# Optimization experiments

Measured on AMD Instinct MI355X. Metric: run time of the kernel, lower is better.

## Reference

```python
import jax, jax.numpy as jnp
import numpy as np

ATOL = 1e-06
RTOL = 1e-06

def setup_inputs() -> dict:
    key = jax.random.key(0)
    ks = jax.random.split(key, 8)
    u = lambda k, shape: jax.random.uniform(k, shape, jnp.float32, -0.05, 0.05)
    return {
        "x": jax.random.normal(ks[0], (4096, 32, 32, 3), jnp.float32),
        "W_lstm": u(ks[1], (3, 16)),      # input kernel, gates [i,f,c,o]
        "U_lstm": u(ks[2], (4, 16)),      # recurrent kernel
        "dw_kernel": u(ks[3], (27, 27, 3, 5)),  # depthwise (kh,kw,in_c,mult)
        "pw_kernel": u(ks[4], (15, 4)),   # pointwise
        "conv_bias": u(ks[5], (4,)),
        "W_td": u(ks[6], (4096, 10)),
        "W_sc": u(ks[7], (4096, 10)),
    }

def _lstm_td(x, W, U):
    # TimeDistributed LSTM: x (B,32,32,3) -> treat axis1 as TD batch, axis2 as time
    B = x.shape[0]
    seq = x.reshape(B * 32, 32, 3)          # (N, T, F)
    xs = jnp.transpose(seq, (1, 0, 2))      # (T, N, F)
    N = seq.shape[0]
    h0 = jnp.zeros((N, 4), x.dtype)
    c0 = jnp.zeros((N, 4), x.dtype)

    def step(carry, xt):
        h, c = carry
        z = xt @ W + h @ U                  # (N, 16)
        zi, zf, zc, zo = jnp.split(z, 4, axis=-1)
        i = jax.nn.elu(zi)                  # recurrent_activation='elu'
        f = jax.nn.elu(zf)
        c = f * c + i * jax.nn.softmax(zc, axis=-1)  # activation='softmax'
        o = jax.nn.elu(zo)
        h = o * jax.nn.softmax(c, axis=-1)
        return (h, c), h

    _, hs = jax.lax.scan(step, (h0, c0), xs)        # (T, N, 4)
    return jnp.transpose(hs, (1, 0, 2)).reshape(B, 32, 32, 4)

def _sep_conv(x, dw_kernel, pw_kernel, conv_bias):
    # depthwise: Keras (kh,kw,C,M) -> lax HWIO grouped (kh,kw,1,C*M), channel-major order
    dw = dw_kernel.reshape(27, 27, 1, 15)
    y = jax.lax.conv_general_dilated(
        x, dw, window_strides=(1, 1), padding='SAME',
        feature_group_count=3,
        dimension_numbers=('NHWC', 'HWIO', 'NHWC'))   # (B,32,32,15)
    y = jnp.einsum('bhwc,cf->bhwf', y, pw_kernel) + conv_bias
    return jax.nn.sigmoid(y)                          # (B,32,32,4)

def reference(x, W_lstm, U_lstm, dw_kernel, pw_kernel, conv_bias, W_td, W_sc):
    B = x.shape[0]
    td = _lstm_td(x, W_lstm, U_lstm).reshape(B, -1) @ W_td   # (B,10)
    sc = _sep_conv(x, dw_kernel, pw_kernel, conv_bias).reshape(B, -1) @ W_sc
    diff = jnp.abs(td - sc)
    tol = ATOL + RTOL * jnp.abs(sc)
    return diff <= tol
```

## Files before the change

kernel.cpp:

```cpp
#include <hip/hip_runtime.h>
#include <math.h>

#define TD_OFF 0
#define WTDR_OFF 40960
#define BG_BYTE_OFF 524288

typedef __bf16 bf16x8 __attribute__((ext_vector_type(8)));
typedef float f32x16 __attribute__((ext_vector_type(16)));

union FragU { bf16x8 v; float4 f; };

__device__ __forceinline__ f32x16 mfma16(bf16x8 a, bf16x8 b, f32x16 c) {
    return __builtin_amdgcn_mfma_f32_32x32x16_bf16(a, b, c, 0, 0, 0);
}

__device__ __forceinline__ float eluf(float v) {
    return v > 0.f ? v : __expf(v) - 1.f;
}

__global__ __launch_bounds__(256) void lstm_prep(const float* __restrict__ x,
                                                 const float* __restrict__ W,
                                                 const float* __restrict__ U,
                                                 const float* __restrict__ Wtd,
                                                 const float* __restrict__ dw,
                                                 const float* __restrict__ pw,
                                                 float* __restrict__ Wtdr,
                                                 unsigned short* __restrict__ Bg,
                                                 float* __restrict__ td_out) {
    int t = threadIdx.x;
    if (blockIdx.x >= 512) {
        int gid = (blockIdx.x - 512) * 256 + t;
        if (gid < 40960) {
            int k = gid & 3;
            int r = gid >> 2;
            int j = r % 10; r /= 10;
            int row = r & 31;
            int tt = r >> 5;
            Wtdr[gid] = Wtd[(size_t)(row * 128 + tt * 4 + k) * 10 + j];
            return;
        }
        int g2 = gid - 40960;
        if (g2 >= 162 * 128) return;
        int n = g2 & 127;
        int s = g2 >> 7;
        int half = s & 1;
        int cd = s >> 1;
        int c = cd / 27, d = cd % 27;
        int w = n >> 2, f = n & 3;
        unsigned short* dsth = Bg + (size_t)s * 4096 + n * 16;
        unsigned short* dstl = dsth + 2048;
#pragma unroll
        for (int k = 0; k < 16; k++) {
            int xi = half * 16 + k;
            int dx = xi - w + 13;
            float v = 0.f;
            if (dx >= 0 && dx < 27) {
#pragma unroll
                for (int m = 0; m < 5; m++)
                    v = fmaf(dw[((d * 27 + dx) * 3 + c) * 5 + m],
                             pw[(c * 5 + m) * 4 + f], v);
            }
            __bf16 h = (__bf16)v;
            __bf16 l = (__bf16)(v - (float)h);
            dsth[k] = __builtin_bit_cast(unsigned short, h);
            dstl[k] = __builtin_bit_cast(unsigned short, l);
        }
        return;
    }

    float rW[48], rU[64];
    const float4* W4 = (const float4*)W;
    const float4* U4 = (const float4*)U;
#pragma unroll
    for (int i = 0; i < 12; i++) {
        float4 q = W4[i];
        rW[i * 4 + 0] = q.x; rW[i * 4 + 1] = q.y;
        rW[i * 4 + 2] = q.z; rW[i * 4 + 3] = q.w;
    }
#pragma unroll
    for (int i = 0; i < 16; i++) {
        float4 q = U4[i];
        rU[i * 4 + 0] = q.x; rU[i * 4 + 1] = q.y;
        rU[i * 4 + 2] = q.z; rU[i * 4 + 3] = q.w;
    }

    int n = blockIdx.x * 256 + t;
    int row = n & 31;
    const float4* xp4 = (const float4*)(x + (size_t)n * 96);

    float h0 = 0, h1 = 0, h2 = 0, h3 = 0;
    float c0 = 0, c1 = 0, c2 = 0, c3 = 0;
    float acc[10];
#pragma unroll
    for (int j = 0; j < 10; j++) acc[j] = 0.f;

    for (int g = 0; g < 8; g++) {
        float4 q0 = xp4[g * 3 + 0], q1 = xp4[g * 3 + 1], q2 = xp4[g * 3 + 2];
        float xr[12] = {q0.x, q0.y, q0.z, q0.w, q1.x, q1.y,
                        q1.z, q1.w, q2.x, q2.y, q2.z, q2.w};
#pragma unroll
        for (int st = 0; st < 4; st++) {
            int tt = g * 4 + st;
            float x0 = xr[st * 3 + 0], x1 = xr[st * 3 + 1], x2 = xr[st * 3 + 2];
            float z[16];
#pragma unroll
            for (int k = 0; k < 16; k++)
                z[k] = x0 * rW[k] + x1 * rW[16 + k] + x2 * rW[32 + k]
                     + h0 * rU[k] + h1 * rU[16 + k] + h2 * rU[32 + k] + h3 * rU[48 + k];

            float ig0 = eluf(z[0]),  ig1 = eluf(z[1]),  ig2 = eluf(z[2]),  ig3 = eluf(z[3]);
            float fg0 = eluf(z[4]),  fg1 = eluf(z[5]),  fg2 = eluf(z[6]),  fg3 = eluf(z[7]);
            float og0 = eluf(z[12]), og1 = eluf(z[13]), og2 = eluf(z[14]), og3 = eluf(z[15]);

            float zm = fmaxf(fmaxf(z[8], z[9]), fmaxf(z[10], z[11]));
            float e0 = __expf(z[8] - zm), e1 = __expf(z[9] - zm);
            float e2 = __expf(z[10] - zm), e3 = __expf(z[11] - zm);
            float inv = 1.f / (e0 + e1 + e2 + e3);
            c0 = fg0 * c0 + ig0 * (e0 * inv);
            c1 = fg1 * c1 + ig1 * (e1 * inv);
            c2 = fg2 * c2 + ig2 * (e2 * inv);
            c3 = fg3 * c3 + ig3 * (e3 * inv);

            float cm = fmaxf(fmaxf(c0, c1), fmaxf(c2, c3));
            float p0 = __expf(c0 - cm), p1 = __expf(c1 - cm);
            float p2 = __expf(c2 - cm), p3 = __expf(c3 - cm);
            float pinv = 1.f / (p0 + p1 + p2 + p3);
            h0 = og0 * (p0 * pinv); h1 = og1 * (p1 * pinv);
            h2 = og2 * (p2 * pinv); h3 = og3 * (p3 * pinv);

            const float4* wr4 = (const float4*)(Wtdr + (size_t)(tt * 32 + row) * 40);
#pragma unroll
            for (int j = 0; j < 10; j++) {
                float4 q = wr4[j];
                acc[j] += h0 * q.x + h1 * q.y + h2 * q.z + h3 * q.w;
            }
        }
    }

#pragma unroll
    for (int off = 16; off >= 1; off >>= 1) {
#pragma unroll
        for (int j = 0; j < 10; j++) acc[j] += __shfl_xor(acc[j], off, 64);
    }
    int lane = t & 63;
    if (lane == 0 || lane == 32) {
        int b = n >> 5;
#pragma unroll
        for (int j = 0; j < 10; j++) td_out[b * 10 + j] = acc[j];
    }
}

#define A_OFF 0
#define ZOFF 24576
#define SRED_OFF 24592
#define LDS_BYTES 24912

__global__ __launch_bounds__(256, 4) void conv_sc(const float* __restrict__ x,
                                                  const unsigned short* __restrict__ Bg,
                                                  const float* __restrict__ Wsc,
                                                  const float* __restrict__ bias,
                                                  const float* __restrict__ td,
                                                  float* __restrict__ out) {
    __shared__ char LDS[LDS_BYTES] __attribute__((aligned(16)));
    int t = threadIdx.x;
    int l = t & 63;
    int wv = t >> 6;
    int m = l & 31;
    int sub = l >> 5;

    const char* bbase = (const char*)Bg + (size_t)wv * 1024 + m * 32 + sub * 16;
    FragU bufA[2], bufB[2], bufC[2];
#define LOADB(sv, arr) { const char* p_ = bbase + (size_t)(sv) * 8192;       \
        arr[0].f = *(const float4*)(p_);                                     \
        arr[1].f = *(const float4*)(p_ + 4096); }

    LOADB(0, bufA);
    LOADB(1, bufB);

    const float4* xb4 = (const float4*)(x + (size_t)blockIdx.x * 6144);
#pragma unroll
    for (int it = 0; it < 6; it++) {
        int fi = it * 256 + t;
        float4 q = xb4[fi];
        float vals[4] = {q.x, q.y, q.z, q.w};
#pragma unroll
        for (int e = 0; e < 4; e++) {
            int pel = fi * 4 + e;
            int img = pel / 3072;
            int p = pel - img * 3072;
            int c = p % 3;
            int hw = p / 3;
            int w = hw & 31;
            int h = hw >> 5;
            int rec = A_OFF + (((img * 3 + c) * 8) + (w >> 4) * 2 + ((w >> 3) & 1)) * 512
                      + h * 16 + (w & 7) * 2;
            float v = vals[e];
            __bf16 hb = (__bf16)v;
            __bf16 lb = (__bf16)(v - (float)hb);
            *(__bf16*)(LDS + rec) = hb;
            *(__bf16*)(LDS + rec + 2048) = lb;
        }
    }
    if (t < 4) *(float*)(LDS + ZOFF + t * 4) = 0.f;
    __syncthreads();

    f32x16 acc0 = {0,0,0,0,0,0,0,0,0,0,0,0,0,0,0,0};
    f32x16 acc1 = acc0;

    int c = 0, d = 0, half = 0;

#define CHUNK(USE, DST, SNEXT) {                                              \
    LOADB(SNEXT, DST);                                                        \
    int rowIdx = m + d - 13;                                                  \
    bool valid = (unsigned)rowIdx < 32u;                                      \
    int a0 = A_OFF + (c * 8 + half * 2 + sub) * 512 + rowIdx * 16;            \
    int ah0o = valid ? a0 : ZOFF;                                             \
    int al0o = valid ? (a0 + 2048) : ZOFF;                                    \
    int ah1o = valid ? (a0 + 12288) : ZOFF;                                   \
    int al1o = valid ? (a0 + 14336) : ZOFF;                                   \
    FragU ah0, al0, ah1, al1;                                                 \
    ah0.f = *(const float4*)(LDS + ah0o);                                     \
    al0.f = *(const float4*)(LDS + al0o);                                     \
    ah1.f = *(const float4*)(LDS + ah1o);                                     \
    al1.f = *(const float4*)(LDS + al1o);                                     \
    acc0 = mfma16(ah0.v, USE[0].v, acc0);                                     \
    acc1 = mfma16(ah1.v, USE[0].v, acc1);                                     \
    acc0 = mfma16(ah0.v, USE[1].v, acc0);                                     \
    acc1 = mfma16(ah1.v, USE[1].v, acc1);                                     \
    acc0 = mfma16(al0.v, USE[0].v, acc0);                                     \
    acc1 = mfma16(al1.v, USE[0].v, acc1);                                     \
    half ^= 1;                                                                \
    if (!half) { d++; if (d == 27) { d = 0; c++; } }                          \
}

    for (int g = 0; g < 54; g++) {
        CHUNK(bufA, bufC, 3 * g + 2);
        CHUNK(bufB, bufA, 3 * g + 3);
        CHUNK(bufC, bufB, 3 * g + 4);
    }

    float b4[4];
#pragma unroll
    for (int i = 0; i < 4; i++) b4[i] = bias[i];

    float part[2][10];
#pragma unroll
    for (int i = 0; i < 2; i++)
#pragma unroll
        for (int j = 0; j < 10; j++) part[i][j] = 0.f;

    f32x16 accs[2] = {acc0, acc1};
#pragma unroll
    for (int i2 = 0; i2 < 2; i2++) {
        int ncol = wv * 32 + m;
        int wcol = ncol >> 2;
        int f = ncol & 3;
        f32x16 a = accs[i2];
#pragma unroll
        for (int r = 0; r < 16; r++) {
            int h = (r & 3) + 8 * (r >> 2) + 4 * sub;
            float v = a[r] + b4[f];
            float sg = 1.f / (1.f + expf(-v));
            const float* wr = Wsc + (size_t)((h * 32 + wcol) * 4 + f) * 10;
#pragma unroll
            for (int j = 0; j < 10; j++) part[i2][j] = fmaf(sg, wr[j], part[i2][j]);
        }
    }

#pragma unroll
    for (int off = 32; off >= 1; off >>= 1) {
#pragma unroll
        for (int i2 = 0; i2 < 2; i2++)
#pragma unroll
            for (int j = 0; j < 10; j++) part[i2][j] += __shfl_xor(part[i2][j], off, 64);
    }
    if (l == 0) {
        float* red = (float*)(LDS + SRED_OFF);
#pragma unroll
        for (int i2 = 0; i2 < 2; i2++)
#pragma unroll
            for (int j = 0; j < 10; j++) red[(wv * 2 + i2) * 10 + j] = part[i2][j];
    }
    __syncthreads();
    if (t < 20) {
        int i2 = t / 10, j = t % 10;
        const float* red = (const float*)(LDS + SRED_OFF);
        float sv = red[(0 * 2 + i2) * 10 + j] + red[(1 * 2 + i2) * 10 + j]
                 + red[(2 * 2 + i2) * 10 + j] + red[(3 * 2 + i2) * 10 + j];
        int oi = (blockIdx.x * 2 + i2) * 10 + j;
        float a = td[oi];
        float tol = 1e-6f + 1e-6f * fabsf(sv);
        out[oi] = (fabsf(a - sv) <= tol) ? 1.0f : 0.0f;
    }
}

extern "C" void kernel_launch(void* const* d_in, const int* in_sizes, int n_in,
                              void* d_out, int out_size, void* d_ws, size_t ws_size,
                              hipStream_t stream) {
    const float* x    = (const float*)d_in[0];
    const float* W    = (const float*)d_in[1];
    const float* U    = (const float*)d_in[2];
    const float* dw   = (const float*)d_in[3];
    const float* pw   = (const float*)d_in[4];
    const float* bias = (const float*)d_in[5];
    const float* Wtd  = (const float*)d_in[6];
    const float* Wsc  = (const float*)d_in[7];

    float* ws     = (float*)d_ws;
    float* td_acc = ws + TD_OFF;
    float* Wtdr   = ws + WTDR_OFF;
    unsigned short* Bg = (unsigned short*)((char*)d_ws + BG_BYTE_OFF);

    lstm_prep<<<753, 256, 0, stream>>>(x, W, U, Wtd, dw, pw, Wtdr, Bg, td_acc);
    conv_sc<<<2048, 256, 0, stream>>>(x, Bg, Wsc, bias, td_acc, (float*)d_out);
}
```

Measured before the change: 400.0 us.

## Split LSTM into own kernel with LDS-staged input and remap conv MFMA tiles

Splits the old fused prep kernel into a weight-prep kernel and a separate LSTM kernel. The LSTM kernel runs 64-thread blocks and stages x through padded LDS, so per-thread strided global loads become coalesced. The conv kernel now gives each wave one image and two N-tiles instead of two images and one N-tile, which halves A-fragment LDS reads per wave. It also moves to double-buffered B loads issued after the MFMAs and raises the launch-bounds occupancy hint from 4 to 5. The trade-offs are an extra launch, a serial dependence between prep and the LSTM, and more B-fragment register and global-load pressure per wave.

Result: slower. 507.6 us (+26.9%).

```diff
diff --git a/kernel.cpp b/kernel.cpp
--- a/kernel.cpp
+++ b/kernel.cpp
@@ -18,55 +18,66 @@
     return v > 0.f ? v : __expf(v) - 1.f;
 }
 
-__global__ __launch_bounds__(256) void lstm_prep(const float* __restrict__ x,
-                                                 const float* __restrict__ W,
-                                                 const float* __restrict__ U,
-                                                 const float* __restrict__ Wtd,
-                                                 const float* __restrict__ dw,
-                                                 const float* __restrict__ pw,
-                                                 float* __restrict__ Wtdr,
-                                                 unsigned short* __restrict__ Bg,
-                                                 float* __restrict__ td_out) {
+__global__ __launch_bounds__(256) void prep(const float* __restrict__ dw,
+                                            const float* __restrict__ pw,
+                                            const float* __restrict__ Wtd,
+                                            float* __restrict__ Wtdr,
+                                            unsigned short* __restrict__ Bg) {
+    int gid = blockIdx.x * 256 + threadIdx.x;
+    if (gid < 40960) {
+        int k = gid & 3;
+        int r = gid >> 2;
+        int j = r % 10; r /= 10;
+        int row = r & 31;
+        int tt = r >> 5;
+        Wtdr[gid] = Wtd[(size_t)(row * 128 + tt * 4 + k) * 10 + j];
+        return;
+    }
+    int g2 = gid - 40960;
+    if (g2 >= 162 * 128) return;
+    int n = g2 & 127;
+    int s = g2 >> 7;
+    int half = s & 1;
+    int cd = s >> 1;
+    int c = cd / 27, d = cd % 27;
+    int w = n >> 2, f = n & 3;
+    unsigned short* dsth = Bg + (size_t)s * 4096 + n * 16;
+    unsigned short* dstl = dsth + 2048;
+#pragma unroll
+    for (int k = 0; k < 16; k++) {
+        int xi = half * 16 + k;
+        int dx = xi - w + 13;
+        float v = 0.f;
+        if (dx >= 0 && dx < 27) {
+#pragma unroll
+            for (int m = 0; m < 5; m++)
+                v = fmaf(dw[((d * 27 + dx) * 3 + c) * 5 + m],
+                         pw[(c * 5 + m) * 4 + f], v);
+        }
+        __bf16 h = (__bf16)v;
+        __bf16 l = (__bf16)(v - (float)h);
+        dsth[k] = __builtin_bit_cast(unsigned short, h);
+        dstl[k] = __builtin_bit_cast(unsigned short, l);
+    }
+}
+
+__global__ __launch_bounds__(64) void lstm_td(const float* __restrict__ x,
+                                              const float* __restrict__ W,
+                                              const float* __restrict__ U,
+                                              const float* __restrict__ Wtdr,
+                                              float* __restrict__ td_out) {
+    __shared__ float4 xls[64 * 25];
     int t = threadIdx.x;
-    if (blockIdx.x >= 512) {
-        int gid = (blockIdx.x - 512) * 256 + t;
-        if (gid < 40960) {
-            int k = gid & 3;
-            int r = gid >> 2;
-            int j = r % 10; r /= 10;
-            int row = r & 31;
-            int tt = r >> 5;
-            Wtdr[gid] = Wtd[(size_t)(row * 128 + tt * 4 + k) * 10 + j];
-            return;
-        }
-        int g2 = gid - 40960;
-        if (g2 >= 162 * 128) return;
-        int n = g2 & 127;
-        int s = g2 >> 7;
-        int half = s & 1;
-        int cd = s >> 1;
-        int c = cd / 27, d = cd % 27;
-        int w = n >> 2, f = n & 3;
-        unsigned short* dsth = Bg + (size_t)s * 4096 + n * 16;
-        unsigned short* dstl = dsth + 2048;
-#pragma unroll
-        for (int k = 0; k < 16; k++) {
-            int xi = half * 16 + k;
-            int dx = xi - w + 13;
-            float v = 0.f;
-            if (dx >= 0 && dx < 27) {
-#pragma unroll
-                for (int m = 0; m < 5; m++)
-                    v = fmaf(dw[((d * 27 + dx) * 3 + c) * 5 + m],
-                             pw[(c * 5 + m) * 4 + f], v);
-            }
-            __bf16 h = (__bf16)v;
-            __bf16 l = (__bf16)(v - (float)h);
-            dsth[k] = __builtin_bit_cast(unsigned short, h);
-            dstl[k] = __builtin_bit_cast(unsigned short, l);
-        }
-        return;
-    }
+
+    const float4* xb4 = (const float4*)(x + (size_t)blockIdx.x * 64 * 96);
+#pragma unroll
+    for (int i = 0; i < 24; i++) {
+        int fidx = i * 64 + t;
+        int seq = fidx / 24;
+        int e = fidx - seq * 24;
+        xls[seq * 25 + e] = xb4[fidx];
+    }
+    __syncthreads();
 
     float rW[48], rU[64];
     const float4* W4 = (const float4*)W;
@@ -84,9 +95,8 @@
         rU[i * 4 + 2] = q.z; rU[i * 4 + 3] = q.w;
     }
 
-    int n = blockIdx.x * 256 + t;
+    int n = blockIdx.x * 64 + t;
     int row = n & 31;
-    const float4* xp4 = (const float4*)(x + (size_t)n * 96);
 
     float h0 = 0, h1 = 0, h2 = 0, h3 = 0;
     float c0 = 0, c1 = 0, c2 = 0, c3 = 0;
@@ -95,7 +105,9 @@
     for (int j = 0; j < 10; j++) acc[j] = 0.f;
 
     for (int g = 0; g < 8; g++) {
-        float4 q0 = xp4[g * 3 + 0], q1 = xp4[g * 3 + 1], q2 = xp4[g * 3 + 2];
+        float4 q0 = xls[t * 25 + g * 3 + 0];
+        float4 q1 = xls[t * 25 + g * 3 + 1];
+        float4 q2 = xls[t * 25 + g * 3 + 2];
         float xr[12] = {q0.x, q0.y, q0.z, q0.w, q1.x, q1.y,
                         q1.z, q1.w, q2.x, q2.y, q2.z, q2.w};
 #pragma unroll
@@ -142,8 +154,7 @@
 #pragma unroll
         for (int j = 0; j < 10; j++) acc[j] += __shfl_xor(acc[j], off, 64);
     }
-    int lane = t & 63;
-    if (lane == 0 || lane == 32) {
+    if (t == 0 || t == 32) {
         int b = n >> 5;
 #pragma unroll
         for (int j = 0; j < 10; j++) td_out[b * 10 + j] = acc[j];
@@ -153,9 +164,9 @@
 #define A_OFF 0
 #define ZOFF 24576
 #define SRED_OFF 24592
-#define LDS_BYTES 24912
-
-__global__ __launch_bounds__(256, 4) void conv_sc(const float* __restrict__ x,
+#define LDS_BYTES 24752
+
+__global__ __launch_bounds__(256, 5) void conv_sc(const float* __restrict__ x,
                                                   const unsigned short* __restrict__ Bg,
                                                   const float* __restrict__ Wsc,
                                                   const float* __restrict__ bias,
@@ -167,12 +178,16 @@
     int wv = t >> 6;
     int m = l & 31;
     int sub = l >> 5;
-
-    const char* bbase = (const char*)Bg + (size_t)wv * 1024 + m * 32 + sub * 16;
-    FragU bufA[2], bufB[2], bufC[2];
+    int img = wv >> 1;
+    int ntbase = (wv & 1) * 2;
+
+    const char* bbase = (const char*)Bg + (size_t)(ntbase * 32 + m) * 32 + sub * 16;
+    FragU bufA[4], bufB[4];
 #define LOADB(sv, arr) { const char* p_ = bbase + (size_t)(sv) * 8192;       \
-        arr[0].f = *(const float4*)(p_);                                     \
-        arr[1].f = *(const float4*)(p_ + 4096); }
+        arr[0].f = *(const float4*)(p_);                         \
+        arr[1].f = *(const float4*)(p_ + 4096);                  \
+        arr[2].f = *(const float4*)(p_ + 1024);                  \
+        arr[3].f = *(const float4*)(p_ + 5120); }
 
     LOADB(0, bufA);
     LOADB(1, bufB);
@@ -186,13 +201,13 @@
 #pragma unroll
         for (int e = 0; e < 4; e++) {
             int pel = fi * 4 + e;
-            int img = pel / 3072;
-            int p = pel - img * 3072;
+            int im = pel / 3072;
+            int p = pel - im * 3072;
             int c = p % 3;
             int hw = p / 3;
             int w = hw & 31;
             int h = hw >> 5;
-            int rec = A_OFF + (((img * 3 + c) * 8) + (w >> 4) * 2 + ((w >> 3) & 1)) * 512
+            int rec = A_OFF + (((im * 3 + c) * 8) + (w >> 4) * 2 + ((w >> 3) & 1)) * 512
                       + h * 16 + (w & 7) * 2;
             float v = vals[e];
             __bf16 hb = (__bf16)v;
@@ -208,54 +223,48 @@
     f32x16 acc1 = acc0;
 
     int c = 0, d = 0, half = 0;
-
-#define CHUNK(USE, DST, SNEXT) {                                              \
-    LOADB(SNEXT, DST);                                                        \
+    int aimg = A_OFF + img * 12288;
+
+#define CHUNK(USE, SNEXT) {                                                   \
     int rowIdx = m + d - 13;                                                  \
     bool valid = (unsigned)rowIdx < 32u;                                      \
-    int a0 = A_OFF + (c * 8 + half * 2 + sub) * 512 + rowIdx * 16;            \
-    int ah0o = valid ? a0 : ZOFF;                                             \
-    int al0o = valid ? (a0 + 2048) : ZOFF;                                    \
-    int ah1o = valid ? (a0 + 12288) : ZOFF;                                   \
-    int al1o = valid ? (a0 + 14336) : ZOFF;                                   \
-    FragU ah0, al0, ah1, al1;                                                 \
-    ah0.f = *(const float4*)(LDS + ah0o);                                     \
-    al0.f = *(const float4*)(LDS + al0o);                                     \
-    ah1.f = *(const float4*)(LDS + ah1o);                                     \
-    al1.f = *(const float4*)(LDS + al1o);                                     \
-    acc0 = mfma16(ah0.v, USE[0].v, acc0);                                     \
-    acc1 = mfma16(ah1.v, USE[0].v, acc1);                                     \
-    acc0 = mfma16(ah0.v, USE[1].v, acc0);                                     \
-    acc1 = mfma16(ah1.v, USE[1].v, acc1);                                     \
-    acc0 = mfma16(al0.v, USE[0].v, acc0);                                     \
-    acc1 = mfma16(al1.v, USE[0].v, acc1);                                     \
+    int a0 = aimg + (c * 8 + half * 2 + sub) * 512 + rowIdx * 16;             \
+    int aho = valid ? a0 : ZOFF;                                              \
+    int alo = valid ? (a0 + 2048) : ZOFF;                                     \
+    FragU ah, al;                                                             \
+    ah.f = *(const float4*)(LDS + aho);                                       \
+    al.f = *(const float4*)(LDS + alo);                                       \
+    acc0 = mfma16(ah.v, USE[0].v, acc0);                                      \
+    acc1 = mfma16(ah.v, USE[2].v, acc1);                                      \
+    acc0 = mfma16(ah.v, USE[1].v, acc0);                                      \
+    acc1 = mfma16(ah.v, USE[3].v, acc1);                                      \
+    acc0 = mfma16(al.v, USE[0].v, acc0);                                      \
+    acc1 = mfma16(al.v, USE[2].v, acc1);                                      \
+    LOADB(SNEXT, USE);                                                        \
     half ^= 1;                                                                \
     if (!half) { d++; if (d == 27) { d = 0; c++; } }                          \
 }
 
-    for (int g = 0; g < 54; g++) {
-        CHUNK(bufA, bufC, 3 * g + 2);
-        CHUNK(bufB, bufA, 3 * g + 3);
-        CHUNK(bufC, bufB, 3 * g + 4);
+    for (int g = 0; g < 81; g++) {
+        CHUNK(bufA, 2 * g + 2);
+        CHUNK(bufB, 2 * g + 3);
     }
 
     float b4[4];
 #pragma unroll
     for (int i = 0; i < 4; i++) b4[i] = bias[i];
 
-    float part[2][10];
-#pragma unroll
-    for (int i = 0; i < 2; i++)
-#pragma unroll
-        for (int j = 0; j < 10; j++) part[i][j] = 0.f;
+    float part[10];
+#pragma unroll
+    for (int j = 0; j < 10; j++) part[j] = 0.f;
 
     f32x16 accs[2] = {acc0, acc1};
 #pragma unroll
-    for (int i2 = 0; i2 < 2; i2++) {
-        int ncol = wv * 32 + m;
+    for (int j2 = 0; j2 < 2; j2++) {
+        int ncol = (ntbase + j2) * 32 + m;
         int wcol = ncol >> 2;
         int f = ncol & 3;
-        f32x16 a = accs[i2];
+        f32x16 a = accs[j2];
 #pragma unroll
         for (int r = 0; r < 16; r++) {
             int h = (r & 3) + 8 * (r >> 2) + 4 * sub;
@@ -263,30 +272,25 @@
             float sg = 1.f / (1.f + expf(-v));
             const float* wr = Wsc + (size_t)((h * 32 + wcol) * 4 + f) * 10;
 #pragma unroll
-            for (int j = 0; j < 10; j++) part[i2][j] = fmaf(sg, wr[j], part[i2][j]);
+            for (int j = 0; j < 10; j++) part[j] = fmaf(sg, wr[j], part[j]);
         }
     }
 
 #pragma unroll
     for (int off = 32; off >= 1; off >>= 1) {
 #pragma unroll
-        for (int i2 = 0; i2 < 2; i2++)
-#pragma unroll
-            for (int j = 0; j < 10; j++) part[i2][j] += __shfl_xor(part[i2][j], off, 64);
+        for (int j = 0; j < 10; j++) part[j] += __shfl_xor(part[j], off, 64);
     }
     if (l == 0) {
         float* red = (float*)(LDS + SRED_OFF);
 #pragma unroll
-        for (int i2 = 0; i2 < 2; i2++)
-#pragma unroll
-            for (int j = 0; j < 10; j++) red[(wv * 2 + i2) * 10 + j] = part[i2][j];
+        for (int j = 0; j < 10; j++) red[wv * 10 + j] = part[j];
     }
     __syncthreads();
     if (t < 20) {
         int i2 = t / 10, j = t % 10;
         const float* red = (const float*)(LDS + SRED_OFF);
-        float sv = red[(0 * 2 + i2) * 10 + j] + red[(1 * 2 + i2) * 10 + j]
-                 + red[(2 * 2 + i2) * 10 + j] + red[(3 * 2 + i2) * 10 + j];
+        float sv = red[(i2 * 2) * 10 + j] + red[(i2 * 2 + 1) * 10 + j];
         int oi = (blockIdx.x * 2 + i2) * 10 + j;
         float a = td[oi];
         float tol = 1e-6f + 1e-6f * fabsf(sv);
@@ -311,6 +315,7 @@
     float* Wtdr   = ws + WTDR_OFF;
     unsigned short* Bg = (unsigned short*)((char*)d_ws + BG_BYTE_OFF);
 
-    lstm_prep<<<753, 256, 0, stream>>>(x, W, U, Wtd, dw, pw, Wtdr, Bg, td_acc);
+    prep<<<241, 256, 0, stream>>>(dw, pw, Wtd, Wtdr, Bg);
+    lstm_td<<<2048, 64, 0, stream>>>(x, W, U, Wtdr, td_acc);
     conv_sc<<<2048, 256, 0, stream>>>(x, Bg, Wsc, bias, td_acc, (float*)d_out);
 }
```

## Run LSTM blocks concurrently with conv blocks in one fused launch

Applied to the files above, without the earlier changes.

Splits the weight-prep work into its own small kernel, then merges the LSTM recurrence blocks and the separable-conv MFMA blocks into one grid so the two independent branches run side by side on the GPU. LSTM weights now come from LDS instead of registers. A third tiny kernel does the final tolerance compare, since the conv blocks can no longer read the LSTM result directly. This adds one extra launch and routes the conv result through global memory, and the LSTM blocks inherit the conv kernel's launch bounds and LDS footprint.

Result: slower. 456.4 us (+14.1%).

```diff
diff --git a/kernel.cpp b/kernel.cpp
--- a/kernel.cpp
+++ b/kernel.cpp
@@ -2,7 +2,8 @@
 #include <math.h>
 
 #define TD_OFF 0
-#define WTDR_OFF 40960
+#define SC_OFF 40960
+#define WTDR_OFF 81920
 #define BG_BYTE_OFF 524288
 
 typedef __bf16 bf16x8 __attribute__((ext_vector_type(8)));
@@ -18,151 +19,141 @@
     return v > 0.f ? v : __expf(v) - 1.f;
 }
 
-__global__ __launch_bounds__(256) void lstm_prep(const float* __restrict__ x,
-                                                 const float* __restrict__ W,
-                                                 const float* __restrict__ U,
-                                                 const float* __restrict__ Wtd,
-                                                 const float* __restrict__ dw,
-                                                 const float* __restrict__ pw,
-                                                 float* __restrict__ Wtdr,
-                                                 unsigned short* __restrict__ Bg,
-                                                 float* __restrict__ td_out) {
-    int t = threadIdx.x;
-    if (blockIdx.x >= 512) {
-        int gid = (blockIdx.x - 512) * 256 + t;
-        if (gid < 40960) {
-            int k = gid & 3;
-            int r = gid >> 2;
-            int j = r % 10; r /= 10;
-            int row = r & 31;
-            int tt = r >> 5;
-            Wtdr[gid] = Wtd[(size_t)(row * 128 + tt * 4 + k) * 10 + j];
-            return;
-        }
-        int g2 = gid - 40960;
-        if (g2 >= 162 * 128) return;
-        int n = g2 & 127;
-        int s = g2 >> 7;
-        int half = s & 1;
-        int cd = s >> 1;
-        int c = cd / 27, d = cd % 27;
-        int w = n >> 2, f = n & 3;
-        unsigned short* dsth = Bg + (size_t)s * 4096 + n * 16;
-        unsigned short* dstl = dsth + 2048;
-#pragma unroll
-        for (int k = 0; k < 16; k++) {
-            int xi = half * 16 + k;
-            int dx = xi - w + 13;
-            float v = 0.f;
-            if (dx >= 0 && dx < 27) {
-#pragma unroll
-                for (int m = 0; m < 5; m++)
-                    v = fmaf(dw[((d * 27 + dx) * 3 + c) * 5 + m],
-                             pw[(c * 5 + m) * 4 + f], v);
-            }
-            __bf16 h = (__bf16)v;
-            __bf16 l = (__bf16)(v - (float)h);
-            dsth[k] = __builtin_bit_cast(unsigned short, h);
-            dstl[k] = __builtin_bit_cast(unsigned short, l);
-        }
+__global__ __launch_bounds__(256) void prep(const float* __restrict__ dw,
+                                            const float* __restrict__ pw,
+                                            const float* __restrict__ Wtd,
+                                            float* __restrict__ Wtdr,
+                                            unsigned short* __restrict__ Bg) {
+    int gid = blockIdx.x * 256 + threadIdx.x;
+    if (gid < 40960) {
+        int k = gid & 3;
+        int r = gid >> 2;
+        int j = r % 10; r /= 10;
+        int row = r & 31;
+        int tt = r >> 5;
+        Wtdr[gid] = Wtd[(size_t)(row * 128 + tt * 4 + k) * 10 + j];
         return;
     }
-
-    float rW[48], rU[64];
-    const float4* W4 = (const float4*)W;
-    const float4* U4 = (const float4*)U;
-#pragma unroll
-    for (int i = 0; i < 12; i++) {
-        float4 q = W4[i];
-        rW[i * 4 + 0] = q.x; rW[i * 4 + 1] = q.y;
-        rW[i * 4 + 2] = q.z; rW[i * 4 + 3] = q.w;
-    }
-#pragma unroll
-    for (int i = 0; i < 16; i++) {
-        float4 q = U4[i];
-        rU[i * 4 + 0] = q.x; rU[i * 4 + 1] = q.y;
-        rU[i * 4 + 2] = q.z; rU[i * 4 + 3] = q.w;
-    }
-
-    int n = blockIdx.x * 256 + t;
-    int row = n & 31;
-    const float4* xp4 = (const float4*)(x + (size_t)n * 96);
-
-    float h0 = 0, h1 = 0, h2 = 0, h3 = 0;
-    float c0 = 0, c1 = 0, c2 = 0, c3 = 0;
-    float acc[10];
-#pragma unroll
-    for (int j = 0; j < 10; j++) acc[j] = 0.f;
-
-    for (int g = 0; g < 8; g++) {
-        float4 q0 = xp4[g * 3 + 0], q1 = xp4[g * 3 + 1], q2 = xp4[g * 3 + 2];
-        float xr[12] = {q0.x, q0.y, q0.z, q0.w, q1.x, q1.y,
-                        q1.z, q1.w, q2.x, q2.y, q2.z, q2.w};
-#pragma unroll
-        for (int st = 0; st < 4; st++) {
-            int tt = g * 4 + st;
-            float x0 = xr[st * 3 + 0], x1 = xr[st * 3 + 1], x2 = xr[st * 3 + 2];
-            float z[16];
-#pragma unroll
-            for (int k = 0; k < 16; k++)
-                z[k] = x0 * rW[k] + x1 * rW[16 + k] + x2 * rW[32 + k]
-                     + h0 * rU[k] + h1 * rU[16 + k] + h2 * rU[32 + k] + h3 * rU[48 + k];
-
-            float ig0 = eluf(z[0]),  ig1 = eluf(z[1]),  ig2 = eluf(z[2]),  ig3 = eluf(z[3]);
-            float fg0 = eluf(z[4]),  fg1 = eluf(z[5]),  fg2 = eluf(z[6]),  fg3 = eluf(z[7]);
-            float og0 = eluf(z[12]), og1 = eluf(z[13]), og2 = eluf(z[14]), og3 = eluf(z[15]);
-
-            float zm = fmaxf(fmaxf(z[8], z[9]), fmaxf(z[10], z[11]));
-            float e0 = __expf(z[8] - zm), e1 = __expf(z[9] - zm);
-            float e2 = __expf(z[10] - zm), e3 = __expf(z[11] - zm);
-            float inv = 1.f / (e0 + e1 + e2 + e3);
-            c0 = fg0 * c0 + ig0 * (e0 * inv);
-            c1 = fg1 * c1 + ig1 * (e1 * inv);
-            c2 = fg2 * c2 + ig2 * (e2 * inv);
-            c3 = fg3 * c3 + ig3 * (e3 * inv);
-
-            float cm = fmaxf(fmaxf(c0, c1), fmaxf(c2, c3));
-            float p0 = __expf(c0 - cm), p1 = __expf(c1 - cm);
-            float p2 = __expf(c2 - cm), p3 = __expf(c3 - cm);
-            float pinv = 1.f / (p0 + p1 + p2 + p3);
-            h0 = og0 * (p0 * pinv); h1 = og1 * (p1 * pinv);
-            h2 = og2 * (p2 * pinv); h3 = og3 * (p3 * pinv);
-
-            const float4* wr4 = (const float4*)(Wtdr + (size_t)(tt * 32 + row) * 40);
-#pragma unroll
-            for (int j = 0; j < 10; j++) {
-                float4 q = wr4[j];
-                acc[j] += h0 * q.x + h1 * q.y + h2 * q.z + h3 * q.w;
-            }
-        }
-    }
-
-#pragma unroll
-    for (int off = 16; off >= 1; off >>= 1) {
-#pragma unroll
-        for (int j = 0; j < 10; j++) acc[j] += __shfl_xor(acc[j], off, 64);
-    }
-    int lane = t & 63;
-    if (lane == 0 || lane == 32) {
-        int b = n >> 5;
-#pragma unroll
-        for (int j = 0; j < 10; j++) td_out[b * 10 + j] = acc[j];
+    int g2 = gid - 40960;
+    if (g2 >= 162 * 128) return;
+    int n = g2 & 127;
+    int s = g2 >> 7;
+    int half = s & 1;
+    int cd = s >> 1;
+    int c = cd / 27, d = cd % 27;
+    int w = n >> 2, f = n & 3;
+    unsigned short* dsth = Bg + (size_t)s * 4096 + n * 16;
+    unsigned short* dstl = dsth + 2048;
+#pragma unroll
+    for (int k = 0; k < 16; k++) {
+        int xi = half * 16 + k;
+        int dx = xi - w + 13;
+        float v = 0.f;
+        if (dx >= 0 && dx < 27) {
+#pragma unroll
+            for (int m = 0; m < 5; m++)
+                v = fmaf(dw[((d * 27 + dx) * 3 + c) * 5 + m],
+                         pw[(c * 5 + m) * 4 + f], v);
+        }
+        __bf16 h = (__bf16)v;
+        __bf16 l = (__bf16)(v - (float)h);
+        dsth[k] = __builtin_bit_cast(unsigned short, h);
+        dstl[k] = __builtin_bit_cast(unsigned short, l);
     }
 }
 
 #define A_OFF 0
 #define ZOFF 24576
 #define SRED_OFF 24592
-#define LDS_BYTES 24912
-
-__global__ __launch_bounds__(256, 4) void conv_sc(const float* __restrict__ x,
-                                                  const unsigned short* __restrict__ Bg,
-                                                  const float* __restrict__ Wsc,
-                                                  const float* __restrict__ bias,
-                                                  const float* __restrict__ td,
-                                                  float* __restrict__ out) {
+#define LDS_BYTES 24752
+
+__global__ __launch_bounds__(256, 4) void fused(const float* __restrict__ x,
+                                                const float* __restrict__ W,
+                                                const float* __restrict__ U,
+                                                const float* __restrict__ Wtdr,
+                                                const unsigned short* __restrict__ Bg,
+                                                const float* __restrict__ Wsc,
+                                                const float* __restrict__ bias,
+                                                float* __restrict__ td_out,
+                                                float* __restrict__ sc_out) {
     __shared__ char LDS[LDS_BYTES] __attribute__((aligned(16)));
     int t = threadIdx.x;
+
+    if (blockIdx.x < 512) {
+        float* sW = (float*)LDS;
+        float* sU = (float*)LDS + 48;
+        if (t < 48) sW[t] = W[t];
+        else if (t < 112) sU[t - 48] = U[t - 48];
+        __syncthreads();
+
+        int n = blockIdx.x * 256 + t;
+        int row = n & 31;
+        const float4* xp4 = (const float4*)(x + (size_t)n * 96);
+
+        float h0 = 0, h1 = 0, h2 = 0, h3 = 0;
+        float c0 = 0, c1 = 0, c2 = 0, c3 = 0;
+        float acc[10];
+#pragma unroll
+        for (int j = 0; j < 10; j++) acc[j] = 0.f;
+
+        for (int g = 0; g < 8; g++) {
+            float4 q0 = xp4[g * 3 + 0], q1 = xp4[g * 3 + 1], q2 = xp4[g * 3 + 2];
+            float xr[12] = {q0.x, q0.y, q0.z, q0.w, q1.x, q1.y,
+                            q1.z, q1.w, q2.x, q2.y, q2.z, q2.w};
+#pragma unroll
+            for (int st = 0; st < 4; st++) {
+                int tt = g * 4 + st;
+                float x0 = xr[st * 3 + 0], x1 = xr[st * 3 + 1], x2 = xr[st * 3 + 2];
+                float z[16];
+#pragma unroll
+                for (int k = 0; k < 16; k++)
+                    z[k] = x0 * sW[k] + x1 * sW[16 + k] + x2 * sW[32 + k]
+                         + h0 * sU[k] + h1 * sU[16 + k] + h2 * sU[32 + k] + h3 * sU[48 + k];
+
+                float ig0 = eluf(z[0]),  ig1 = eluf(z[1]),  ig2 = eluf(z[2]),  ig3 = eluf(z[3]);
+                float fg0 = eluf(z[4]),  fg1 = eluf(z[5]),  fg2 = eluf(z[6]),  fg3 = eluf(z[7]);
+                float og0 = eluf(z[12]), og1 = eluf(z[13]), og2 = eluf(z[14]), og3 = eluf(z[15]);
+
+                float zm = fmaxf(fmaxf(z[8], z[9]), fmaxf(z[10], z[11]));
+                float e0 = __expf(z[8] - zm), e1 = __expf(z[9] - zm);
+                float e2 = __expf(z[10] - zm), e3 = __expf(z[11] - zm);
+                float inv = 1.f / (e0 + e1 + e2 + e3);
+                c0 = fg0 * c0 + ig0 * (e0 * inv);
+                c1 = fg1 * c1 + ig1 * (e1 * inv);
+                c2 = fg2 * c2 + ig2 * (e2 * inv);
+                c3 = fg3 * c3 + ig3 * (e3 * inv);
+
+                float cm = fmaxf(fmaxf(c0, c1), fmaxf(c2, c3));
+                float p0 = __expf(c0 - cm), p1 = __expf(c1 - cm);
+                float p2 = __expf(c2 - cm), p3 = __expf(c3 - cm);
+                float pinv = 1.f / (p0 + p1 + p2 + p3);
+                h0 = og0 * (p0 * pinv); h1 = og1 * (p1 * pinv);
+                h2 = og2 * (p2 * pinv); h3 = og3 * (p3 * pinv);
+
+                const float4* wr4 = (const float4*)(Wtdr + (size_t)(tt * 32 + row) * 40);
+#pragma unroll
+                for (int j = 0; j < 10; j++) {
+                    float4 q = wr4[j];
+                    acc[j] += h0 * q.x + h1 * q.y + h2 * q.z + h3 * q.w;
+                }
+            }
+        }
+
+#pragma unroll
+        for (int off = 16; off >= 1; off >>= 1) {
+#pragma unroll
+            for (int j = 0; j < 10; j++) acc[j] += __shfl_xor(acc[j], off, 64);
+        }
+        int lane = t & 63;
+        if (lane == 0 || lane == 32) {
+            int b = n >> 5;
+#pragma unroll
+            for (int j = 0; j < 10; j++) td_out[b * 10 + j] = acc[j];
+        }
+        return;
+    }
+
+    int bid = blockIdx.x - 512;
     int l = t & 63;
     int wv = t >> 6;
     int m = l & 31;
@@ -177,7 +168,7 @@
     LOADB(0, bufA);
     LOADB(1, bufB);
 
-    const float4* xb4 = (const float4*)(x + (size_t)blockIdx.x * 6144);
+    const float4* xb4 = (const float4*)(x + (size_t)bid * 6144);
 #pragma unroll
     for (int it = 0; it < 6; it++) {
         int fi = it * 256 + t;
@@ -186,13 +177,13 @@
 #pragma unroll
         for (int e = 0; e < 4; e++) {
             int pel = fi * 4 + e;
-            int img = pel / 3072;
-            int p = pel - img * 3072;
+            int im = pel / 3072;
+            int p = pel - im * 3072;
             int c = p % 3;
             int hw = p / 3;
             int w = hw & 31;
             int h = hw >> 5;
-            int rec = A_OFF + (((img * 3 + c) * 8) + (w >> 4) * 2 + ((w >> 3) & 1)) * 512
+            int rec = A_OFF + (((im * 3 + c) * 8) + (w >> 4) * 2 + ((w >> 3) & 1)) * 512
                       + h * 16 + (w & 7) * 2;
             float v = vals[e];
             __bf16 hb = (__bf16)v;
@@ -287,10 +278,18 @@
         const float* red = (const float*)(LDS + SRED_OFF);
         float sv = red[(0 * 2 + i2) * 10 + j] + red[(1 * 2 + i2) * 10 + j]
                  + red[(2 * 2 + i2) * 10 + j] + red[(3 * 2 + i2) * 10 + j];
-        int oi = (blockIdx.x * 2 + i2) * 10 + j;
-        float a = td[oi];
-        float tol = 1e-6f + 1e-6f * fabsf(sv);
-        out[oi] = (fabsf(a - sv) <= tol) ? 1.0f : 0.0f;
+        sc_out[(bid * 2 + i2) * 10 + j] = sv;
+    }
+}
+
+__global__ __launch_bounds__(256) void finalize(const float* __restrict__ td,
+                                                const float* __restrict__ sc,
+                                                float* __restrict__ out, int n) {
+    int i = blockIdx.x * 256 + threadIdx.x;
+    if (i < n) {
+        float a = td[i], s = sc[i];
+        float tol = 1e-6f + 1e-6f * fabsf(s);
+        out[i] = (fabsf(a - s) <= tol) ? 1.0f : 0.0f;
     }
 }
 
@@ -308,9 +307,11 @@
 
     float* ws     = (float*)d_ws;
     float* td_acc = ws + TD_OFF;
+    float* sc_acc = ws + SC_OFF;
     float* Wtdr   = ws + WTDR_OFF;
     unsigned short* Bg = (unsigned short*)((char*)d_ws + BG_BYTE_OFF);
 
-    lstm_prep<<<753, 256, 0, stream>>>(x, W, U, Wtd, dw, pw, Wtdr, Bg, td_acc);
-    conv_sc<<<2048, 256, 0, stream>>>(x, Bg, Wsc, bias, td_acc, (float*)d_out);
-}
+    prep<<<241, 256, 0, stream>>>(dw, pw, Wtd, Wtdr, Bg);
+    fused<<<2560, 256, 0, stream>>>(x, W, U, Wtdr, Bg, Wsc, bias, td_acc, sc_acc);
+    finalize<<<(out_size + 255) / 256, 256, 0, stream>>>(td_acc, sc_acc, (float*)d_out, out_size);
+}
```

## Split prep from LSTM kernel and stage LSTM inputs through shared memory

Applied to the files above, without the earlier changes.

The weight-reformatting work moves into its own prep kernel, and the LSTM becomes a separate kernel. That kernel loads its block's input slab cooperatively into padded LDS in four chunks, so the global loads are coalesced instead of each thread reading its own strided 384-byte row. This adds block barriers and an extra kernel launch. It also makes the LSTM depend on Wtdr through stream ordering, which fixes a possible race in the old fused layout where prep blocks wrote Wtdr while LSTM blocks were reading it.

Measured after the change: 430.4 us. 1.08x slower.

```diff
diff --git a/kernel.cpp b/kernel.cpp
--- a/kernel.cpp
+++ b/kernel.cpp
@@ -18,55 +18,56 @@
     return v > 0.f ? v : __expf(v) - 1.f;
 }
 
-__global__ __launch_bounds__(256) void lstm_prep(const float* __restrict__ x,
-                                                 const float* __restrict__ W,
-                                                 const float* __restrict__ U,
-                                                 const float* __restrict__ Wtd,
-                                                 const float* __restrict__ dw,
-                                                 const float* __restrict__ pw,
-                                                 float* __restrict__ Wtdr,
-                                                 unsigned short* __restrict__ Bg,
-                                                 float* __restrict__ td_out) {
+__global__ __launch_bounds__(256) void prep(const float* __restrict__ dw,
+                                            const float* __restrict__ pw,
+                                            const float* __restrict__ Wtd,
+                                            float* __restrict__ Wtdr,
+                                            unsigned short* __restrict__ Bg) {
+    int gid = blockIdx.x * 256 + threadIdx.x;
+    if (gid < 40960) {
+        int k = gid & 3;
+        int r = gid >> 2;
+        int j = r % 10; r /= 10;
+        int row = r & 31;
+        int tt = r >> 5;
+        Wtdr[gid] = Wtd[(size_t)(row * 128 + tt * 4 + k) * 10 + j];
+        return;
+    }
+    int g2 = gid - 40960;
+    if (g2 >= 162 * 128) return;
+    int n = g2 & 127;
+    int s = g2 >> 7;
+    int half = s & 1;
+    int cd = s >> 1;
+    int c = cd / 27, d = cd % 27;
+    int w = n >> 2, f = n & 3;
+    unsigned short* dsth = Bg + (size_t)s * 4096 + n * 16;
+    unsigned short* dstl = dsth + 2048;
+#pragma unroll
+    for (int k = 0; k < 16; k++) {
+        int xi = half * 16 + k;
+        int dx = xi - w + 13;
+        float v = 0.f;
+        if (dx >= 0 && dx < 27) {
+#pragma unroll
+            for (int m = 0; m < 5; m++)
+                v = fmaf(dw[((d * 27 + dx) * 3 + c) * 5 + m],
+                         pw[(c * 5 + m) * 4 + f], v);
+        }
+        __bf16 h = (__bf16)v;
+        __bf16 l = (__bf16)(v - (float)h);
+        dsth[k] = __builtin_bit_cast(unsigned short, h);
+        dstl[k] = __builtin_bit_cast(unsigned short, l);
+    }
+}
+
+__global__ void lstm_td(const float* __restrict__ x,
+                        const float* __restrict__ W,
+                        const float* __restrict__ U,
+                        const float* __restrict__ Wtdr,
+                        float* __restrict__ td_out) {
+    __shared__ float xs[256 * 25];
     int t = threadIdx.x;
-    if (blockIdx.x >= 512) {
-        int gid = (blockIdx.x - 512) * 256 + t;
-        if (gid < 40960) {
-            int k = gid & 3;
-            int r = gid >> 2;
-            int j = r % 10; r /= 10;
-            int row = r & 31;
-            int tt = r >> 5;
-            Wtdr[gid] = Wtd[(size_t)(row * 128 + tt * 4 + k) * 10 + j];
-            return;
-        }
-        int g2 = gid - 40960;
-        if (g2 >= 162 * 128) return;
-        int n = g2 & 127;
-        int s = g2 >> 7;
-        int half = s & 1;
-        int cd = s >> 1;
-        int c = cd / 27, d = cd % 27;
-        int w = n >> 2, f = n & 3;
-        unsigned short* dsth = Bg + (size_t)s * 4096 + n * 16;
-        unsigned short* dstl = dsth + 2048;
-#pragma unroll
-        for (int k = 0; k < 16; k++) {
-            int xi = half * 16 + k;
-            int dx = xi - w + 13;
-            float v = 0.f;
-            if (dx >= 0 && dx < 27) {
-#pragma unroll
-                for (int m = 0; m < 5; m++)
-                    v = fmaf(dw[((d * 27 + dx) * 3 + c) * 5 + m],
-                             pw[(c * 5 + m) * 4 + f], v);
-            }
-            __bf16 h = (__bf16)v;
-            __bf16 l = (__bf16)(v - (float)h);
-            dsth[k] = __builtin_bit_cast(unsigned short, h);
-            dstl[k] = __builtin_bit_cast(unsigned short, l);
-        }
-        return;
-    }
 
     float rW[48], rU[64];
     const float4* W4 = (const float4*)W;
@@ -86,7 +87,7 @@
 
     int n = blockIdx.x * 256 + t;
     int row = n & 31;
-    const float4* xp4 = (const float4*)(x + (size_t)n * 96);
+    const float4* xb4 = (const float4*)(x + (size_t)blockIdx.x * 24576);
 
     float h0 = 0, h1 = 0, h2 = 0, h3 = 0;
     float c0 = 0, c1 = 0, c2 = 0, c3 = 0;
@@ -94,14 +95,25 @@
 #pragma unroll
     for (int j = 0; j < 10; j++) acc[j] = 0.f;
 
-    for (int g = 0; g < 8; g++) {
-        float4 q0 = xp4[g * 3 + 0], q1 = xp4[g * 3 + 1], q2 = xp4[g * 3 + 2];
-        float xr[12] = {q0.x, q0.y, q0.z, q0.w, q1.x, q1.y,
-                        q1.z, q1.w, q2.x, q2.y, q2.z, q2.w};
-#pragma unroll
-        for (int st = 0; st < 4; st++) {
-            int tt = g * 4 + st;
-            float x0 = xr[st * 3 + 0], x1 = xr[st * 3 + 1], x2 = xr[st * 3 + 2];
+    for (int c4 = 0; c4 < 4; c4++) {
+        __syncthreads();
+#pragma unroll
+        for (int it = 0; it < 6; it++) {
+            int fi = it * 256 + t;
+            int s = fi / 6, e = fi - s * 6;
+            float4 q = xb4[s * 24 + c4 * 6 + e];
+            int base = s * 25 + e * 4;
+            xs[base + 0] = q.x; xs[base + 1] = q.y;
+            xs[base + 2] = q.z; xs[base + 3] = q.w;
+        }
+        __syncthreads();
+
+#pragma unroll
+        for (int st = 0; st < 8; st++) {
+            int tt = c4 * 8 + st;
+            float x0 = xs[t * 25 + st * 3 + 0];
+            float x1 = xs[t * 25 + st * 3 + 1];
+            float x2 = xs[t * 25 + st * 3 + 2];
             float z[16];
 #pragma unroll
             for (int k = 0; k < 16; k++)
@@ -186,13 +198,13 @@
 #pragma unroll
         for (int e = 0; e < 4; e++) {
             int pel = fi * 4 + e;
-            int img = pel / 3072;
-            int p = pel - img * 3072;
+            int im = pel / 3072;
+            int p = pel - im * 3072;
             int c = p % 3;
             int hw = p / 3;
             int w = hw & 31;
             int h = hw >> 5;
-            int rec = A_OFF + (((img * 3 + c) * 8) + (w >> 4) * 2 + ((w >> 3) & 1)) * 512
+            int rec = A_OFF + (((im * 3 + c) * 8) + (w >> 4) * 2 + ((w >> 3) & 1)) * 512
                       + h * 16 + (w & 7) * 2;
             float v = vals[e];
             __bf16 hb = (__bf16)v;
@@ -311,6 +323,7 @@
     float* Wtdr   = ws + WTDR_OFF;
     unsigned short* Bg = (unsigned short*)((char*)d_ws + BG_BYTE_OFF);
 
-    lstm_prep<<<753, 256, 0, stream>>>(x, W, U, Wtd, dw, pw, Wtdr, Bg, td_acc);
+    prep<<<241, 256, 0, stream>>>(dw, pw, Wtd, Wtdr, Bg);
+    lstm_td<<<512, 256, 0, stream>>>(x, W, U, Wtdr, td_acc);
     conv_sc<<<2048, 256, 0, stream>>>(x, Bg, Wsc, bias, td_acc, (float*)d_out);
 }
```
